# Kernel tuning notes

Hardware: AMD Instinct MI355X
Metric: run time of the kernel (lower is better)

Reference implementation:

```python
import jax, jax.numpy as jnp
import numpy as np

LARGE_CONSTANT = 1e9


def setup_inputs() -> dict:
    key = jax.random.key(0)
    ks = jax.random.split(key, 8)
    B, S, D, U = 8, 2048, 1024, 1024
    scale = 1.0 / np.sqrt(D)
    inputs_1 = jax.random.normal(ks[0], (B, S, D), dtype=jnp.float32)
    inputs_2 = jax.random.normal(ks[1], (B, S, D), dtype=jnp.float32)
    Wq = jax.random.normal(ks[2], (D, U), dtype=jnp.float32) * scale
    Wk = jax.random.normal(ks[3], (D, U), dtype=jnp.float32) * scale
    Wv = jax.random.normal(ks[4], (D, U), dtype=jnp.float32) * scale
    bq = jnp.zeros((U,), dtype=jnp.float32)
    bk = jnp.zeros((U,), dtype=jnp.float32)
    bv = jnp.zeros((U,), dtype=jnp.float32)
    # metric initialized as identity in the original; add small noise to exercise it
    metric = jnp.eye(U, dtype=jnp.float32) + 0.01 * jax.random.normal(ks[5], (U, U), dtype=jnp.float32)
    return {"inputs_1": inputs_1, "inputs_2": inputs_2, "Wq": Wq, "bq": bq,
            "Wk": Wk, "bk": bk, "Wv": Wv, "bv": bv, "metric": metric}


def reference(inputs_1, inputs_2, Wq, bq, Wk, bk, Wv, bv, metric):
    U = Wq.shape[1]
    scaling = jnp.sqrt(jnp.asarray(U, dtype=inputs_1.dtype))
    queries = inputs_1 @ Wq + bq            # [b, i, u]
    keys = inputs_2 @ Wk + bk               # [b, j, u]
    values = inputs_2 @ Wv + bv             # [b, j, u]
    queries = jnp.einsum('biu,uv->biv', queries, metric)  # learned-metric transform
    scores = jnp.einsum('biu,bju->bij', queries, keys) / scaling
    # causal mask: band_part(ones, -1, 0) is lower-triangular
    S = scores.shape[-1]
    causal = jnp.tril(jnp.ones((S, S), dtype=scores.dtype))
    scores = scores - LARGE_CONSTANT * (1.0 - causal)
    alpha = jax.nn.softmax(scores, axis=-1)
    return jnp.einsum('bij,bju->biu', alpha, values)
```

## Files before the change

kernel.cpp:

```cpp
#include <hip/hip_runtime.h>


#define Bq 8
#define Sq 2048
#define Dq 1024
#define Uq 1024

typedef __bf16 bf16;
typedef __bf16 bf16x8 __attribute__((ext_vector_type(8)));
typedef float f32x4 __attribute__((ext_vector_type(4)));
typedef unsigned short u16;
typedef unsigned int u32;

__device__ __forceinline__ u16 f2bf(float f) {
  u32 u = __builtin_bit_cast(u32, f);
  u32 r = u + 0x7fffu + ((u >> 16) & 1u);
  return (u16)(r >> 16);
}
__device__ __forceinline__ float bf2f(u32 h) {
  return __builtin_bit_cast(float, h << 16);
}

__device__ __forceinline__ void gl_lds16(const void* g, void* l) {
  __builtin_amdgcn_global_load_lds(
      (const __attribute__((address_space(1))) u32*)g,
      (__attribute__((address_space(3))) u32*)l, 16, 0, 0);
}


__global__ __launch_bounds__(256) void cvt_bf16(const float* __restrict__ in,
                                                u16* __restrict__ out, int n4) {
  int idx = blockIdx.x * 256 + threadIdx.x;
  if (idx >= n4) return;
  float4 v = ((const float4*)in)[idx];
  ushort4 o;
  o.x = f2bf(v.x); o.y = f2bf(v.y); o.z = f2bf(v.z); o.w = f2bf(v.w);
  ((ushort4*)out)[idx] = o;
}

__global__ __launch_bounds__(256) void transpose_cvt(const float* __restrict__ in,
                                                     u16* __restrict__ out, int N) {
  __shared__ float tile[32][33];
  int tx = threadIdx.x & 31, ty = threadIdx.x >> 5;
  int x0 = blockIdx.x * 32, y0 = blockIdx.y * 32;
#pragma unroll
  for (int r = 0; r < 32; r += 8)
    tile[ty + r][tx] = in[(size_t)(y0 + ty + r) * N + x0 + tx];
  __syncthreads();
#pragma unroll
  for (int r = 0; r < 32; r += 8)
    out[(size_t)(x0 + ty + r) * N + y0 + tx] = f2bf(tile[tx][ty + r]);
}

__global__ __launch_bounds__(256) void bqm_kernel(const float* __restrict__ bq,
                                                  const float* __restrict__ metric,
                                                  float* __restrict__ bqm) {
  int v = blockIdx.x * 256 + threadIdx.x;
  float s = 0.f;
  for (int u = 0; u < Uq; ++u) s += bq[u] * metric[(size_t)u * Uq + v];
  bqm[v] = s;
}

__global__ __launch_bounds__(256) void fill_zero(float4* __restrict__ p, int n4) {
  int i = blockIdx.x * 256 + threadIdx.x;
  if (i < n4) p[i] = float4{0.f, 0.f, 0.f, 0.f};
}

#define BM 128
#define BN 128
#define BK 32

template <int OUT_BF16, int BIAS>
__global__ __launch_bounds__(256) void gemm_tn(
    const bf16* __restrict__ A, const bf16* __restrict__ B, void* __restrict__ Cv,
    const float* __restrict__ bias, int lda, int ldb, int ldc,
    long long sA, long long sB, long long sC, int K,
    int causal_skip, int causal_klimit) {
  __shared__ __align__(16) bf16 lA[BM * BK];
  __shared__ __align__(16) bf16 lB[BN * BK];
  int m0 = blockIdx.x * BM, n0 = blockIdx.y * BN;
  if (causal_skip && n0 > m0 + BM - 1) return;
  long long b = blockIdx.z;
  A += b * sA;
  B += b * sB;
  int t = threadIdx.x;
  int w = t >> 6, l = t & 63;
  int wr = (w >> 1) * 64, wc = (w & 1) * 64;
  int Kend = causal_klimit ? min(K, m0 + BM) : K;
  int nk = Kend / BK;

  f32x4 acc[4][4] = {};
  int rowA = t >> 2, kc = (t & 3) * 8;
  char* lAb = (char*)lA + w * 1024;
  char* lBb = (char*)lB + w * 1024;
  int lm = l & 15, q = l >> 4;

  for (int kt = 0; kt < nk; ++kt) {
    int k0 = kt * BK;
    const bf16* ga0 = A + (long long)(m0 + rowA) * lda + k0 + kc;
    const bf16* gb0 = B + (long long)(n0 + rowA) * ldb + k0 + kc;
    gl_lds16(ga0, lAb);
    gl_lds16(ga0 + (long long)64 * lda, lAb + 4096);
    gl_lds16(gb0, lBb);
    gl_lds16(gb0 + (long long)64 * ldb, lBb + 4096);
    __syncthreads();
    bf16x8 af[4], bfr[4];
#pragma unroll
    for (int i = 0; i < 4; ++i)
      af[i] = *(const bf16x8*)&lA[(wr + i * 16 + lm) * BK + q * 8];
#pragma unroll
    for (int i = 0; i < 4; ++i)
      bfr[i] = *(const bf16x8*)&lB[(wc + i * 16 + lm) * BK + q * 8];
#pragma unroll
    for (int i = 0; i < 4; ++i)
#pragma unroll
      for (int j = 0; j < 4; ++j)
        acc[i][j] = __builtin_amdgcn_mfma_f32_16x16x32_bf16(af[i], bfr[j], acc[i][j], 0, 0, 0);
    __syncthreads();
  }

  char* Cb = (char*)Cv + (OUT_BF16 ? b * sC * 2 : b * sC * 4);
#pragma unroll
  for (int i = 0; i < 4; ++i) {
#pragma unroll
    for (int j = 0; j < 4; ++j) {
      int col = n0 + wc + j * 16 + lm;
      float bc = (BIAS == 1) ? bias[col] : 0.f;
#pragma unroll
      for (int r = 0; r < 4; ++r) {
        int row = m0 + wr + i * 16 + q * 4 + r;
        float v = acc[i][j][r] + bc;
        if (BIAS == 2) v += bias[row];
        size_t idx = (size_t)row * ldc + col;
        if (OUT_BF16)
          ((u16*)Cb)[idx] = f2bf(v);
        else
          ((float*)Cb)[idx] = v;
      }
    }
  }
}

__global__ __launch_bounds__(256) void softmax_causal(u16* __restrict__ sc) {
  __shared__ __align__(16) float sm[Sq];
  __shared__ float red[8];
  int gr = blockIdx.x;
  int i = gr & (Sq - 1);
  u16* rowp = sc + (size_t)gr * Sq;
  int t = threadIdx.x;
  uint4 pk = ((const uint4*)rowp)[t];
  float4 lo, hi;
  lo.x = bf2f(pk.x & 0xffffu); lo.y = bf2f(pk.x >> 16);
  lo.z = bf2f(pk.y & 0xffffu); lo.w = bf2f(pk.y >> 16);
  hi.x = bf2f(pk.z & 0xffffu); hi.y = bf2f(pk.z >> 16);
  hi.z = bf2f(pk.w & 0xffffu); hi.w = bf2f(pk.w >> 16);
  ((float4*)sm)[2 * t] = lo;
  ((float4*)sm)[2 * t + 1] = hi;
  __syncthreads();
  int nv = i + 1;
  const float scl = 0.03125f;
  float m = -1e30f;
  for (int j = t; j < nv; j += 256) m = fmaxf(m, sm[j]);
#pragma unroll
  for (int o = 32; o; o >>= 1) m = fmaxf(m, __shfl_xor(m, o));
  if ((t & 63) == 0) red[t >> 6] = m;
  __syncthreads();
  m = fmaxf(fmaxf(red[0], red[1]), fmaxf(red[2], red[3])) * scl;
  float sum = 0.f;
  for (int j = t; j < nv; j += 256) sum += __expf(sm[j] * scl - m);
#pragma unroll
  for (int o = 32; o; o >>= 1) sum += __shfl_xor(sum, o);
  if ((t & 63) == 0) red[4 + (t >> 6)] = sum;
  __syncthreads();
  float rinv = 1.0f / (red[4] + red[5] + red[6] + red[7]);
  int j0 = t * 8;
  u16 ov[8];
#pragma unroll
  for (int k = 0; k < 8; ++k)
    ov[k] = (j0 + k < nv) ? f2bf(__expf(sm[j0 + k] * scl - m) * rinv) : (u16)0;
  uint4 po;
  po.x = (u32)ov[0] | ((u32)ov[1] << 16);
  po.y = (u32)ov[2] | ((u32)ov[3] << 16);
  po.z = (u32)ov[4] | ((u32)ov[5] << 16);
  po.w = (u32)ov[6] | ((u32)ov[7] << 16);
  ((uint4*)rowp)[t] = po;
}


extern "C" void kernel_launch(void* const* d_in, const int* in_sizes, int n_in,
                              void* d_out, int out_size, void* d_ws, size_t ws_size,
                              hipStream_t stream) {
  const float* X1 = (const float*)d_in[0];
  const float* X2 = (const float*)d_in[1];
  const float* Wq = (const float*)d_in[2];
  const float* bq = (const float*)d_in[3];
  const float* Wk = (const float*)d_in[4];
  const float* bk = (const float*)d_in[5];
  const float* Wv = (const float*)d_in[6];
  const float* bv = (const float*)d_in[7];
  const float* metric = (const float*)d_in[8];
  float* out = (float*)d_out;

  const size_t XB = (size_t)Bq * Sq * Dq * 2;
  const size_t WB = (size_t)Dq * Uq * 2;
  const size_t NEED = 3 * XB + 5 * WB + 4096;

  if (ws_size < NEED) {
    fill_zero<<<(out_size / 4 + 255) / 256, 256, 0, stream>>>((float4*)d_out, out_size / 4);
    return;
  }

  char* ws = (char*)d_ws;
  bf16* X1b = (bf16*)(ws);
  bf16* X2b = (bf16*)(ws + XB);
  bf16* Vt = (bf16*)(ws + 2 * XB);
  bf16* WqB = (bf16*)(ws + 3 * XB);
  bf16* metT = (bf16*)(ws + 3 * XB + WB);
  bf16* WkT = (bf16*)(ws + 3 * XB + 2 * WB);
  bf16* WvT = (bf16*)(ws + 3 * XB + 3 * WB);
  bf16* WqmT = (bf16*)(ws + 3 * XB + 4 * WB);
  float* bqm = (float*)(ws + 3 * XB + 5 * WB);
  u16* Sc = (u16*)ws;
  bf16* Qb = (bf16*)d_out;
  bf16* Kb = (bf16*)d_out + (size_t)Bq * Sq * Uq;

  cvt_bf16<<<(Bq * Sq * Dq / 4 + 255) / 256, 256, 0, stream>>>(X1, (u16*)X1b, Bq * Sq * Dq / 4);
  cvt_bf16<<<(Bq * Sq * Dq / 4 + 255) / 256, 256, 0, stream>>>(X2, (u16*)X2b, Bq * Sq * Dq / 4);
  cvt_bf16<<<(Dq * Uq / 4 + 255) / 256, 256, 0, stream>>>(Wq, (u16*)WqB, Dq * Uq / 4);
  dim3 tg(32, 32);
  transpose_cvt<<<tg, 256, 0, stream>>>(metric, (u16*)metT, Uq);
  transpose_cvt<<<tg, 256, 0, stream>>>(Wk, (u16*)WkT, Dq);
  transpose_cvt<<<tg, 256, 0, stream>>>(Wv, (u16*)WvT, Dq);
  bqm_kernel<<<Uq / 256, 256, 0, stream>>>(bq, metric, bqm);

  gemm_tn<1, 0><<<dim3(Uq / BM, Dq / BN, 1), 256, 0, stream>>>(
      metT, WqB, WqmT, nullptr, Uq, Uq, Dq, 0, 0, 0, Uq, 0, 0);

  const int MQ = Bq * Sq;
  gemm_tn<1, 1><<<dim3(MQ / BM, Uq / BN, 1), 256, 0, stream>>>(
      X1b, WqmT, Qb, bqm, Dq, Dq, Uq, 0, 0, 0, Dq, 0, 0);
  gemm_tn<1, 1><<<dim3(MQ / BM, Uq / BN, 1), 256, 0, stream>>>(
      X2b, WkT, Kb, bk, Dq, Dq, Uq, 0, 0, 0, Dq, 0, 0);
  gemm_tn<1, 2><<<dim3(Uq / BM, Sq / BN, Bq), 256, 0, stream>>>(
      WvT, X2b, Vt, bv, Dq, Dq, Sq, 0, (long long)Sq * Dq, (long long)Uq * Sq, Dq, 0, 0);

  gemm_tn<1, 0><<<dim3(Sq / BM, Sq / BN, Bq), 256, 0, stream>>>(
      Qb, Kb, Sc, nullptr, Uq, Uq, Sq, (long long)Sq * Uq, (long long)Sq * Uq,
      (long long)Sq * Sq, Uq, 1, 0);

  softmax_causal<<<Bq * Sq, 256, 0, stream>>>(Sc);

  gemm_tn<0, 0><<<dim3(Sq / BM, Uq / BN, Bq), 256, 0, stream>>>(
      (const bf16*)Sc, Vt, out, nullptr, Sq, Sq, Uq, (long long)Sq * Sq,
      (long long)Uq * Sq, (long long)Sq * Uq, Sq, 0, 1);

  (void)in_sizes; (void)n_in; (void)ws_size;
}
```

Baseline: 649.6 us.

## Double-buffer GEMM LDS tiles, reverse causal block order, batch small prep kernels

The GEMM now double-buffers its A/B LDS tiles. It issues the next tile's global-to-LDS loads before computing the current one and uses explicit vmcnt waits and barriers, so load latency overlaps with MFMA work. Causal-limited launches iterate row blocks in reverse so the longest blocks start first. The two input conversions and the three transpose conversions are merged into single launches to cut launch overhead. LDS use doubles, which may reduce occupancy, and the hand-written waitcnt makes correctness depend on the exact load count.

```diff
diff --git a/kernel.cpp b/kernel.cpp
--- a/kernel.cpp
+++ b/kernel.cpp
@@ -27,6 +27,20 @@
       (__attribute__((address_space(3))) u32*)l, 16, 0, 0);
 }
 
+
+__global__ __launch_bounds__(256) void cvt_x(const float* __restrict__ x1,
+                                             const float* __restrict__ x2,
+                                             u16* __restrict__ o1,
+                                             u16* __restrict__ o2, int n4) {
+  int idx = blockIdx.x * 256 + threadIdx.x;
+  if (idx >= n4) return;
+  const float* in = blockIdx.y ? x2 : x1;
+  u16* out = blockIdx.y ? o2 : o1;
+  float4 v = ((const float4*)in)[idx];
+  ushort4 o;
+  o.x = f2bf(v.x); o.y = f2bf(v.y); o.z = f2bf(v.z); o.w = f2bf(v.w);
+  ((ushort4*)out)[idx] = o;
+}
 
 __global__ __launch_bounds__(256) void cvt_bf16(const float* __restrict__ in,
                                                 u16* __restrict__ out, int n4) {
@@ -38,9 +52,14 @@
   ((ushort4*)out)[idx] = o;
 }
 
-__global__ __launch_bounds__(256) void transpose_cvt(const float* __restrict__ in,
-                                                     u16* __restrict__ out, int N) {
+__global__ __launch_bounds__(256) void transpose_cvt3(
+    const float* __restrict__ s0, u16* __restrict__ d0,
+    const float* __restrict__ s1, u16* __restrict__ d1,
+    const float* __restrict__ s2, u16* __restrict__ d2) {
   __shared__ float tile[32][33];
+  const float* in = (blockIdx.z == 0) ? s0 : (blockIdx.z == 1) ? s1 : s2;
+  u16* out = (blockIdx.z == 0) ? d0 : (blockIdx.z == 1) ? d1 : d2;
+  const int N = 1024;
   int tx = threadIdx.x & 31, ty = threadIdx.x >> 5;
   int x0 = blockIdx.x * 32, y0 = blockIdx.y * 32;
 #pragma unroll
@@ -76,9 +95,10 @@
     const float* __restrict__ bias, int lda, int ldb, int ldc,
     long long sA, long long sB, long long sC, int K,
     int causal_skip, int causal_klimit) {
-  __shared__ __align__(16) bf16 lA[BM * BK];
-  __shared__ __align__(16) bf16 lB[BN * BK];
-  int m0 = blockIdx.x * BM, n0 = blockIdx.y * BN;
+  __shared__ __align__(16) bf16 lA[2][BM * BK];
+  __shared__ __align__(16) bf16 lB[2][BN * BK];
+  int bx = causal_klimit ? (gridDim.x - 1 - blockIdx.x) : blockIdx.x;
+  int m0 = bx * BM, n0 = blockIdx.y * BN;
   if (causal_skip && n0 > m0 + BM - 1) return;
   long long b = blockIdx.z;
   A += b * sA;
@@ -91,32 +111,44 @@
 
   f32x4 acc[4][4] = {};
   int rowA = t >> 2, kc = (t & 3) * 8;
-  char* lAb = (char*)lA + w * 1024;
-  char* lBb = (char*)lB + w * 1024;
   int lm = l & 15, q = l >> 4;
 
+  const bf16* gA = A + (long long)(m0 + rowA) * lda + kc;
+  const bf16* gB = B + (long long)(n0 + rowA) * ldb + kc;
+  long long a64 = (long long)64 * lda, b64 = (long long)64 * ldb;
+
+  auto stage = [&](int kt, int buf) {
+    int k0 = kt * BK;
+    char* dA = (char*)lA[buf] + w * 1024;
+    char* dB = (char*)lB[buf] + w * 1024;
+    gl_lds16(gA + k0, dA);
+    gl_lds16(gA + k0 + a64, dA + 4096);
+    gl_lds16(gB + k0, dB);
+    gl_lds16(gB + k0 + b64, dB + 4096);
+  };
+
+  stage(0, 0);
   for (int kt = 0; kt < nk; ++kt) {
-    int k0 = kt * BK;
-    const bf16* ga0 = A + (long long)(m0 + rowA) * lda + k0 + kc;
-    const bf16* gb0 = B + (long long)(n0 + rowA) * ldb + k0 + kc;
-    gl_lds16(ga0, lAb);
-    gl_lds16(ga0 + (long long)64 * lda, lAb + 4096);
-    gl_lds16(gb0, lBb);
-    gl_lds16(gb0 + (long long)64 * ldb, lBb + 4096);
-    __syncthreads();
+    int cur = kt & 1;
+    if (kt + 1 < nk) {
+      stage(kt + 1, cur ^ 1);
+      asm volatile("s_waitcnt vmcnt(4)\n\ts_barrier" ::: "memory");
+    } else {
+      asm volatile("s_waitcnt vmcnt(0)\n\ts_barrier" ::: "memory");
+    }
     bf16x8 af[4], bfr[4];
 #pragma unroll
     for (int i = 0; i < 4; ++i)
-      af[i] = *(const bf16x8*)&lA[(wr + i * 16 + lm) * BK + q * 8];
+      af[i] = *(const bf16x8*)&lA[cur][(wr + i * 16 + lm) * BK + q * 8];
 #pragma unroll
     for (int i = 0; i < 4; ++i)
-      bfr[i] = *(const bf16x8*)&lB[(wc + i * 16 + lm) * BK + q * 8];
+      bfr[i] = *(const bf16x8*)&lB[cur][(wc + i * 16 + lm) * BK + q * 8];
 #pragma unroll
     for (int i = 0; i < 4; ++i)
 #pragma unroll
       for (int j = 0; j < 4; ++j)
         acc[i][j] = __builtin_amdgcn_mfma_f32_16x16x32_bf16(af[i], bfr[j], acc[i][j], 0, 0, 0);
-    __syncthreads();
+    asm volatile("s_barrier" ::: "memory");
   }
 
   char* Cb = (char*)Cv + (OUT_BF16 ? b * sC * 2 : b * sC * 4);
@@ -224,13 +256,11 @@
   bf16* Qb = (bf16*)d_out;
   bf16* Kb = (bf16*)d_out + (size_t)Bq * Sq * Uq;
 
-  cvt_bf16<<<(Bq * Sq * Dq / 4 + 255) / 256, 256, 0, stream>>>(X1, (u16*)X1b, Bq * Sq * Dq / 4);
-  cvt_bf16<<<(Bq * Sq * Dq / 4 + 255) / 256, 256, 0, stream>>>(X2, (u16*)X2b, Bq * Sq * Dq / 4);
+  int nx4 = Bq * Sq * Dq / 4;
+  cvt_x<<<dim3((nx4 + 255) / 256, 2), 256, 0, stream>>>(X1, X2, (u16*)X1b, (u16*)X2b, nx4);
   cvt_bf16<<<(Dq * Uq / 4 + 255) / 256, 256, 0, stream>>>(Wq, (u16*)WqB, Dq * Uq / 4);
-  dim3 tg(32, 32);
-  transpose_cvt<<<tg, 256, 0, stream>>>(metric, (u16*)metT, Uq);
-  transpose_cvt<<<tg, 256, 0, stream>>>(Wk, (u16*)WkT, Dq);
-  transpose_cvt<<<tg, 256, 0, stream>>>(Wv, (u16*)WvT, Dq);
+  transpose_cvt3<<<dim3(32, 32, 3), 256, 0, stream>>>(
+      metric, (u16*)metT, Wk, (u16*)WkT, Wv, (u16*)WvT);
   bqm_kernel<<<Uq / 256, 256, 0, stream>>>(bq, metric, bqm);
 
   gemm_tn<1, 0><<<dim3(Uq / BM, Dq / BN, 1), 256, 0, stream>>>(
```

Result: faster. 601.8 us (-7.4%).
